# Kernel optimization log

Measured on AMD Instinct MI355X. Metric: run time of the kernel, lower is better.

Reference implementation:

```python
import jax, jax.numpy as jnp
import numpy as np

EMBED_DIM = 1024
NUM_HEADS = 16
HEAD_DIM = EMBED_DIM // NUM_HEADS
B, S = 2, 2048


def setup_inputs() -> dict:
    key = jax.random.key(0)
    ks = jax.random.split(key, 10)
    inp = {
        "query": jax.random.normal(ks[0], (B, S, EMBED_DIM), dtype=jnp.float32),
        "key": jax.random.normal(ks[1], (B, S, EMBED_DIM), dtype=jnp.float32),
        "value": jax.random.normal(ks[2], (B, S, EMBED_DIM), dtype=jnp.float32),
        # 0 => masked key position (matches attn_mask == 0 in the torch code)
        "attn_mask": jax.random.randint(ks[3], (B, S), 0, 2, dtype=jnp.int32),
        "Wq": jax.random.normal(ks[4], (EMBED_DIM, EMBED_DIM), dtype=jnp.float32) * 0.02,
        "bq": jnp.zeros((EMBED_DIM,), dtype=jnp.float32),
        "Wk": jax.random.normal(ks[5], (EMBED_DIM, EMBED_DIM), dtype=jnp.float32) * 0.02,
        "bk": jnp.zeros((EMBED_DIM,), dtype=jnp.float32),
        "Wv": jax.random.normal(ks[6], (EMBED_DIM, EMBED_DIM), dtype=jnp.float32) * 0.02,
        "bv": jnp.zeros((EMBED_DIM,), dtype=jnp.float32),
    }
    return inp


def _proj_heads(x, W, b):
    # x: [B, S, E] -> [B, H, S, D]  (nn.Linear uses x @ W.T + b)
    y = x @ W.T + b
    Bx, Sx, E = y.shape
    return y.reshape(Bx, Sx, NUM_HEADS, HEAD_DIM).transpose(0, 2, 1, 3)


def reference(query, key, value, attn_mask, Wq, bq, Wk, bk, Wv, bv):
    q = _proj_heads(query, Wq, bq)   # [B,H,S,D]
    k = _proj_heads(key, Wk, bk)     # [B,H,S,D]
    v = _proj_heads(value, Wv, bv)   # [B,H,S,D]
    inv_scale = float(EMBED_DIM) ** 0.5  # NOTE: original divides by sqrt(embed_dim), not sqrt(head_dim)
    scores = jnp.einsum("bhqd,bhkd->bhqk", q, k) / inv_scale  # [B,H,S,S]
    mask = (attn_mask == 0)[:, None, None, :]  # [B,1,1,S] -> broadcast over [B,H,S,S]
    scores = jnp.where(mask, -jnp.inf, scores)
    attn = jax.nn.softmax(scores, axis=-1)
    # dropout omitted for deterministic reference (see notes)
    out = jnp.einsum("bhqk,bhkd->bhqd", attn, v)  # [B,H,S,D]
    return out
```

## Files before the change

kernel.cpp:

```cpp
#include <hip/hip_runtime.h>
#include <hip/hip_bf16.h>

constexpr int BB = 2;
constexpr int SS = 2048;
constexpr int EE = 1024;
constexpr int HH = 16;
constexpr int DD = 64;
constexpr int MM = BB * SS;
constexpr int CX = MM * EE;
constexpr int CW = EE * EE;
#define QSCALE 0.045084220027780106f
#define NEGBIG -1e30f

typedef __attribute__((ext_vector_type(8))) short short8;
typedef __attribute__((ext_vector_type(4))) float floatx4;

__device__ inline short bf16bits(float x) {
    __hip_bfloat16 h = __float2bfloat16(x);
    return *reinterpret_cast<short*>(&h);
}

__device__ inline unsigned pkbf(float a, float b) {
    return (unsigned)(unsigned short)bf16bits(a) |
           ((unsigned)(unsigned short)bf16bits(b) << 16);
}

__device__ inline float fast_exp2(float x) {
#if __has_builtin(__builtin_amdgcn_exp2f)
    return __builtin_amdgcn_exp2f(x);
#else
    return exp2f(x);
#endif
}

__device__ inline void gl_lds16(const __hip_bfloat16* g, const short* l) {
    __builtin_amdgcn_global_load_lds(
        (const __attribute__((address_space(1))) void*)g,
        (__attribute__((address_space(3))) void*)l, 16, 0, 0);
}

__global__ __launch_bounds__(256) void convert_kernel(
    const float* __restrict__ x0, const float* __restrict__ x1, const float* __restrict__ x2,
    const float* __restrict__ w0, const float* __restrict__ w1, const float* __restrict__ w2,
    __hip_bfloat16* __restrict__ xb, __hip_bfloat16* __restrict__ wb)
{
    const long long e = (long long)(blockIdx.x * 256 + threadIdx.x) * 8;
    const float* src;
    __hip_bfloat16* dst;
    if (e < 3LL * CX) {
        const int z = (int)(e >> 22);
        const int off = (int)(e & (CX - 1));
        src = ((z == 0) ? x0 : (z == 1) ? x1 : x2) + off;
        dst = xb + e;
    } else {
        const long long e2 = e - 3LL * CX;
        const int z = (int)(e2 >> 20);
        const int off = (int)(e2 & (CW - 1));
        src = ((z == 0) ? w0 : (z == 1) ? w1 : w2) + off;
        dst = wb + e2;
    }
    const float4 a = reinterpret_cast<const float4*>(src)[0];
    const float4 b = reinterpret_cast<const float4*>(src)[1];
    short8 r;
    r[0] = bf16bits(a.x); r[1] = bf16bits(a.y); r[2] = bf16bits(a.z); r[3] = bf16bits(a.w);
    r[4] = bf16bits(b.x); r[5] = bf16bits(b.y); r[6] = bf16bits(b.z); r[7] = bf16bits(b.w);
    *reinterpret_cast<short8*>(dst) = r;
}

__global__ __launch_bounds__(256) void proj_gemm(
    const __hip_bfloat16* __restrict__ xb,
    const __hip_bfloat16* __restrict__ wb,
    const float* __restrict__ bq, const float* __restrict__ bk, const float* __restrict__ bv,
    __hip_bfloat16* __restrict__ qws,
    __hip_bfloat16* __restrict__ kws,
    __hip_bfloat16* __restrict__ vtws)
{
    const int which = blockIdx.z;
    const __hip_bfloat16* A = xb + (size_t)which * CX;
    const __hip_bfloat16* W = wb + (size_t)which * CW;
    const float* bias = (which == 0) ? bq : (which == 1) ? bk : bv;

    const int m0   = blockIdx.x * 128;
    const int n0   = blockIdx.y * 128;
    const int tid  = threadIdx.x;
    const int wave = tid >> 6;
    const int lane = tid & 63;
    const int l15  = lane & 15;
    const int quad = lane >> 4;
    const int wr   = wave >> 1;
    const int wc   = wave & 1;

    __shared__ __align__(16) short As[128 * 32];
    __shared__ __align__(16) short Bs[128 * 32];

    const int dpos  = (lane & 7) ^ (lane >> 3);
    const int drloc = 2 * (lane >> 3) + (dpos >> 2);
    const int dgran = (dpos & 3) * 8;

    const int rbase = (l15 >> 1) * 64;
    const int rslot = (((l15 & 1) * 4 + quad) ^ (l15 >> 1)) * 8;

    floatx4 acc[4][4] = {};

    for (int k0 = 0; k0 < EE; k0 += 32) {
        __syncthreads();
        #pragma unroll
        for (int p = 0; p < 2; ++p) {
            const int rb16 = wave * 32 + p * 16;
            gl_lds16(A + (size_t)(m0 + rb16 + drloc) * EE + k0 + dgran, &As[rb16 * 32]);
            gl_lds16(W + (size_t)(n0 + rb16 + drloc) * EE + k0 + dgran, &Bs[rb16 * 32]);
        }
        __syncthreads();

        short8 af[4], bf[4];
        #pragma unroll
        for (int mt = 0; mt < 4; ++mt)
            af[mt] = *reinterpret_cast<const short8*>(
                &As[(wr * 32 + mt * 8) * 64 + rbase + rslot]);
        #pragma unroll
        for (int nt = 0; nt < 4; ++nt)
            bf[nt] = *reinterpret_cast<const short8*>(
                &Bs[(wc * 32 + nt * 8) * 64 + rbase + rslot]);

        #pragma unroll
        for (int mt = 0; mt < 4; ++mt)
            #pragma unroll
            for (int nt = 0; nt < 4; ++nt)
                acc[mt][nt] = __builtin_amdgcn_mfma_f32_16x16x32_bf16(af[mt], bf[nt], acc[mt][nt], 0, 0, 0);
    }

    #pragma unroll
    for (int nt = 0; nt < 4; ++nt) {
        const int n = n0 + wc * 64 + nt * 16 + l15;
        const float bval = bias[n];
        const int h = n >> 6, d = n & 63;
        #pragma unroll
        for (int mt = 0; mt < 4; ++mt) {
            #pragma unroll
            for (int r = 0; r < 4; ++r) {
                const int m = m0 + wr * 64 + mt * 16 + quad * 4 + r;
                const int b = m >> 11;
                const int s = m & (SS - 1);
                float val = acc[mt][nt][r] + bval;
                if (which == 0) val *= QSCALE;
                const __hip_bfloat16 hv = __float2bfloat16(val);
                if (which == 0)
                    qws[(((size_t)b * HH + h) * SS + s) * DD + d] = hv;
                else if (which == 1)
                    kws[(((size_t)b * HH + h) * SS + s) * DD + d] = hv;
                else
                    vtws[(((size_t)b * HH + h) * DD + d) * SS + s] = hv;
            }
        }
    }
}

__global__ __launch_bounds__(256) void attn_kernel(
    const __hip_bfloat16* __restrict__ qws,
    const __hip_bfloat16* __restrict__ kws,
    const __hip_bfloat16* __restrict__ vtws,
    const int* __restrict__ amask,
    float* __restrict__ out)
{
    const int flatb = blockIdx.y * gridDim.x + blockIdx.x;
    const int bh    = 4 * (flatb & 7) + ((flatb >> 3) & 3);
    const int b     = bh >> 4;
    const int q0    = (flatb >> 5) * 64;
    const int tid  = threadIdx.x;
    const int wave = tid >> 6;
    const int lane = tid & 63;
    const int l15  = lane & 15;
    const int quad = lane >> 4;

    const __hip_bfloat16* Q  = qws  + (size_t)bh * SS * DD;
    const __hip_bfloat16* K  = kws  + (size_t)bh * SS * DD;
    const __hip_bfloat16* VT = vtws + (size_t)bh * DD * SS;
    const int* msk = amask + b * SS;

    __shared__ __align__(16) short Ks[64 * 64];
    __shared__ __align__(16) short Vs[64 * 64];
    __shared__ __align__(16) short Ps[4][16 * 64];
    short* pw = Ps[wave];

    const int qrow = q0 + wave * 16 + l15;
    const short8 qa0 = *reinterpret_cast<const short8*>(Q + (size_t)qrow * DD + quad * 8);
    const short8 qa1 = *reinterpret_cast<const short8*>(Q + (size_t)qrow * DD + 32 + quad * 8);

    const int swz = l15 & 7;

    const int srow = lane >> 3;
    const int sg   = ((lane & 7) ^ srow) * 8;

    float l_lane = 0.f;
    floatx4 acc[4] = {};

    for (int kt = 0; kt < SS; kt += 64) {
        __syncthreads();

        #pragma unroll
        for (int p = 0; p < 2; ++p) {
            const int rb = wave * 16 + p * 8;
            gl_lds16(K + (size_t)(kt + rb + srow) * DD + sg, &Ks[rb * 64]);
            gl_lds16(VT + (size_t)(rb + srow) * SS + kt + sg, &Vs[rb * 64]);
        }
        __syncthreads();

        floatx4 st[4];
        #pragma unroll
        for (int f = 0; f < 4; ++f) {
            const int krow = (f * 16 + l15) * 64;
            const short8 ka = *reinterpret_cast<const short8*>(&Ks[krow + (quad ^ swz) * 8]);
            const short8 kb = *reinterpret_cast<const short8*>(&Ks[krow + ((quad + 4) ^ swz) * 8]);
            floatx4 z = {};
            z = __builtin_amdgcn_mfma_f32_16x16x32_bf16(ka, qa0, z, 0, 0, 0);
            z = __builtin_amdgcn_mfma_f32_16x16x32_bf16(kb, qa1, z, 0, 0, 0);
            st[f] = z;
        }

        #pragma unroll
        for (int f = 0; f < 4; ++f) {
            const int4 mi = *reinterpret_cast<const int4*>(msk + kt + f * 16 + quad * 4);
            st[f][0] = fast_exp2(st[f][0] + (mi.x ? 0.f : NEGBIG));
            st[f][1] = fast_exp2(st[f][1] + (mi.y ? 0.f : NEGBIG));
            st[f][2] = fast_exp2(st[f][2] + (mi.z ? 0.f : NEGBIG));
            st[f][3] = fast_exp2(st[f][3] + (mi.w ? 0.f : NEGBIG));
            l_lane += st[f][0] + st[f][1] + st[f][2] + st[f][3];
        }

        #pragma unroll
        for (int f = 0; f < 4; ++f) {
            const int slot = (2 * f + (quad >> 1)) ^ swz;
            uint2 pk;
            pk.x = pkbf(st[f][0], st[f][1]);
            pk.y = pkbf(st[f][2], st[f][3]);
            *reinterpret_cast<uint2*>(pw + l15 * 64 + slot * 8 + (quad & 1) * 4) = pk;
        }
        __asm__ volatile("s_waitcnt lgkmcnt(0)" ::: "memory");

        const short8 pa0 = *reinterpret_cast<const short8*>(pw + l15 * 64 + (quad ^ swz) * 8);
        const short8 pa1 = *reinterpret_cast<const short8*>(pw + l15 * 64 + ((quad + 4) ^ swz) * 8);

        #pragma unroll
        for (int nt = 0; nt < 4; ++nt) {
            const int vrow = (nt * 16 + l15) * 64;
            const short8 vb0 = *reinterpret_cast<const short8*>(&Vs[vrow + (quad ^ swz) * 8]);
            const short8 vb1 = *reinterpret_cast<const short8*>(&Vs[vrow + ((quad + 4) ^ swz) * 8]);
            acc[nt] = __builtin_amdgcn_mfma_f32_16x16x32_bf16(pa0, vb0, acc[nt], 0, 0, 0);
            acc[nt] = __builtin_amdgcn_mfma_f32_16x16x32_bf16(pa1, vb1, acc[nt], 0, 0, 0);
        }
    }

    l_lane += __shfl_xor(l_lane, 16, 64);
    l_lane += __shfl_xor(l_lane, 32, 64);
    float lq[4];
    #pragma unroll
    for (int r = 0; r < 4; ++r)
        lq[r] = __shfl(l_lane, quad * 4 + r, 16);

    const size_t obase = (size_t)bh * SS * DD;
    #pragma unroll
    for (int nt = 0; nt < 4; ++nt)
        #pragma unroll
        for (int r = 0; r < 4; ++r) {
            const int qq = q0 + wave * 16 + quad * 4 + r;
            const int d  = nt * 16 + l15;
            out[obase + (size_t)qq * DD + d] = acc[nt][r] / lq[r];
        }
}

extern "C" void kernel_launch(void* const* d_in, const int* in_sizes, int n_in,
                              void* d_out, int out_size, void* d_ws, size_t ws_size,
                              hipStream_t stream) {
    const float* q    = (const float*)d_in[0];
    const float* k    = (const float*)d_in[1];
    const float* v    = (const float*)d_in[2];
    const int*   mask = (const int*)d_in[3];
    const float* Wq   = (const float*)d_in[4];
    const float* bq   = (const float*)d_in[5];
    const float* Wk   = (const float*)d_in[6];
    const float* bk   = (const float*)d_in[7];
    const float* Wv   = (const float*)d_in[8];
    const float* bv   = (const float*)d_in[9];
    float* out = (float*)d_out;

    __hip_bfloat16* qws  = (__hip_bfloat16*)d_ws;
    __hip_bfloat16* kws  = qws + (size_t)CX;
    __hip_bfloat16* vtws = kws + (size_t)CX;
    __hip_bfloat16* xb   = vtws + (size_t)CX;
    __hip_bfloat16* wb   = xb + (size_t)3 * CX;

    const int cvt_blocks = (3 * CX + 3 * CW) / (256 * 8);
    convert_kernel<<<dim3(cvt_blocks), 256, 0, stream>>>(q, k, v, Wq, Wk, Wv, xb, wb);
    proj_gemm<<<dim3(MM / 128, EE / 128, 3), 256, 0, stream>>>(
        xb, wb, bq, bk, bv, qws, kws, vtws);
    attn_kernel<<<dim3(SS / 64, BB * HH), 256, 0, stream>>>(
        qws, kws, vtws, mask, out);
}
```

Baseline: 215.1 us.

## Double-buffer K/V tiles, widen attention block to 128 queries, precompute mask in LDS

The attention kernel now handles 128 query rows per block, with each wave owning 32 rows, so every K/V tile loaded into LDS is reused twice as much and the grid is halved. K and V tiles are double-buffered, so the next tile's global-to-LDS copy overlaps compute on the current one, with one barrier per iteration instead of two. The mask is converted once to floats in LDS and applied as a multiply after exp2 instead of a select with a large negative bias, and setprio hints are added around the MFMA sections. In exchange the kernel uses more LDS and registers per block and launches fewer blocks, which may lower occupancy.

```diff
diff --git a/kernel.cpp b/kernel.cpp
--- a/kernel.cpp
+++ b/kernel.cpp
@@ -10,7 +10,6 @@
 constexpr int CX = MM * EE;
 constexpr int CW = EE * EE;
 #define QSCALE 0.045084220027780106f
-#define NEGBIG -1e30f
 
 typedef __attribute__((ext_vector_type(8))) short short8;
 typedef __attribute__((ext_vector_type(4))) float floatx4;
@@ -165,7 +164,7 @@
     const int flatb = blockIdx.y * gridDim.x + blockIdx.x;
     const int bh    = 4 * (flatb & 7) + ((flatb >> 3) & 3);
     const int b     = bh >> 4;
-    const int q0    = (flatb >> 5) * 64;
+    const int q0    = (flatb >> 5) * 128;
     const int tid  = threadIdx.x;
     const int wave = tid >> 6;
     const int lane = tid & 63;
@@ -177,94 +176,140 @@
     const __hip_bfloat16* VT = vtws + (size_t)bh * DD * SS;
     const int* msk = amask + b * SS;
 
-    __shared__ __align__(16) short Ks[64 * 64];
-    __shared__ __align__(16) short Vs[64 * 64];
-    __shared__ __align__(16) short Ps[4][16 * 64];
-    short* pw = Ps[wave];
-
-    const int qrow = q0 + wave * 16 + l15;
+    __shared__ __align__(16) short Ks[2][64 * 64];
+    __shared__ __align__(16) short Vs[2][64 * 64];
+    __shared__ __align__(16) short Ps[4][32 * 64];
+    __shared__ __align__(16) float Ms[SS];
+    short* pw0 = Ps[wave];
+    short* pw1 = Ps[wave] + 16 * 64;
+
+    #pragma unroll
+    for (int i = 0; i < 2; ++i) {
+        const int j = tid + i * 256;
+        const int4 m4 = reinterpret_cast<const int4*>(msk)[j];
+        float4 f4;
+        f4.x = (float)m4.x; f4.y = (float)m4.y; f4.z = (float)m4.z; f4.w = (float)m4.w;
+        reinterpret_cast<float4*>(Ms)[j] = f4;
+    }
+
+    const int qrow = q0 + wave * 32 + l15;
     const short8 qa0 = *reinterpret_cast<const short8*>(Q + (size_t)qrow * DD + quad * 8);
     const short8 qa1 = *reinterpret_cast<const short8*>(Q + (size_t)qrow * DD + 32 + quad * 8);
+    const short8 qa2 = *reinterpret_cast<const short8*>(Q + (size_t)(qrow + 16) * DD + quad * 8);
+    const short8 qa3 = *reinterpret_cast<const short8*>(Q + (size_t)(qrow + 16) * DD + 32 + quad * 8);
 
     const int swz = l15 & 7;
 
     const int srow = lane >> 3;
     const int sg   = ((lane & 7) ^ srow) * 8;
 
-    float l_lane = 0.f;
-    floatx4 acc[4] = {};
-
-    for (int kt = 0; kt < SS; kt += 64) {
-        __syncthreads();
-
-        #pragma unroll
-        for (int p = 0; p < 2; ++p) {
-            const int rb = wave * 16 + p * 8;
-            gl_lds16(K + (size_t)(kt + rb + srow) * DD + sg, &Ks[rb * 64]);
-            gl_lds16(VT + (size_t)(rb + srow) * SS + kt + sg, &Vs[rb * 64]);
-        }
-        __syncthreads();
-
-        floatx4 st[4];
+    float l0 = 0.f, l1 = 0.f;
+    floatx4 acc0[4] = {}, acc1[4] = {};
+
+    #pragma unroll
+    for (int p = 0; p < 2; ++p) {
+        const int rb = wave * 16 + p * 8;
+        gl_lds16(K + (size_t)(rb + srow) * DD + sg, &Ks[0][rb * 64]);
+        gl_lds16(VT + (size_t)(rb + srow) * SS + sg, &Vs[0][rb * 64]);
+    }
+    __asm__ volatile("s_waitcnt vmcnt(0) lgkmcnt(0)" ::: "memory");
+    __builtin_amdgcn_s_barrier();
+
+    for (int t = 0; t < SS / 64; ++t) {
+        const int cur = t & 1;
+
+        if (t + 1 < SS / 64) {
+            const int kn = (t + 1) * 64;
+            #pragma unroll
+            for (int p = 0; p < 2; ++p) {
+                const int rb = wave * 16 + p * 8;
+                gl_lds16(K + (size_t)(kn + rb + srow) * DD + sg, &Ks[cur ^ 1][rb * 64]);
+                gl_lds16(VT + (size_t)(rb + srow) * SS + kn + sg, &Vs[cur ^ 1][rb * 64]);
+            }
+        }
+        const int kt = t * 64;
+
+        floatx4 s0[4], s1[4];
+        __builtin_amdgcn_s_setprio(1);
         #pragma unroll
         for (int f = 0; f < 4; ++f) {
             const int krow = (f * 16 + l15) * 64;
-            const short8 ka = *reinterpret_cast<const short8*>(&Ks[krow + (quad ^ swz) * 8]);
-            const short8 kb = *reinterpret_cast<const short8*>(&Ks[krow + ((quad + 4) ^ swz) * 8]);
+            const short8 ka = *reinterpret_cast<const short8*>(&Ks[cur][krow + (quad ^ swz) * 8]);
+            const short8 kb = *reinterpret_cast<const short8*>(&Ks[cur][krow + ((quad + 4) ^ swz) * 8]);
             floatx4 z = {};
             z = __builtin_amdgcn_mfma_f32_16x16x32_bf16(ka, qa0, z, 0, 0, 0);
             z = __builtin_amdgcn_mfma_f32_16x16x32_bf16(kb, qa1, z, 0, 0, 0);
-            st[f] = z;
-        }
+            s0[f] = z;
+            floatx4 w = {};
+            w = __builtin_amdgcn_mfma_f32_16x16x32_bf16(ka, qa2, w, 0, 0, 0);
+            w = __builtin_amdgcn_mfma_f32_16x16x32_bf16(kb, qa3, w, 0, 0, 0);
+            s1[f] = w;
+        }
+        __builtin_amdgcn_s_setprio(0);
 
         #pragma unroll
         for (int f = 0; f < 4; ++f) {
-            const int4 mi = *reinterpret_cast<const int4*>(msk + kt + f * 16 + quad * 4);
-            st[f][0] = fast_exp2(st[f][0] + (mi.x ? 0.f : NEGBIG));
-            st[f][1] = fast_exp2(st[f][1] + (mi.y ? 0.f : NEGBIG));
-            st[f][2] = fast_exp2(st[f][2] + (mi.z ? 0.f : NEGBIG));
-            st[f][3] = fast_exp2(st[f][3] + (mi.w ? 0.f : NEGBIG));
-            l_lane += st[f][0] + st[f][1] + st[f][2] + st[f][3];
-        }
-
-        #pragma unroll
-        for (int f = 0; f < 4; ++f) {
-            const int slot = (2 * f + (quad >> 1)) ^ swz;
-            uint2 pk;
-            pk.x = pkbf(st[f][0], st[f][1]);
-            pk.y = pkbf(st[f][2], st[f][3]);
-            *reinterpret_cast<uint2*>(pw + l15 * 64 + slot * 8 + (quad & 1) * 4) = pk;
+            const float4 mf = *reinterpret_cast<const float4*>(&Ms[kt + f * 16 + quad * 4]);
+            const float e00 = fast_exp2(s0[f][0]) * mf.x;
+            const float e01 = fast_exp2(s0[f][1]) * mf.y;
+            const float e02 = fast_exp2(s0[f][2]) * mf.z;
+            const float e03 = fast_exp2(s0[f][3]) * mf.w;
+            const float e10 = fast_exp2(s1[f][0]) * mf.x;
+            const float e11 = fast_exp2(s1[f][1]) * mf.y;
+            const float e12 = fast_exp2(s1[f][2]) * mf.z;
+            const float e13 = fast_exp2(s1[f][3]) * mf.w;
+            l0 += e00 + e01 + e02 + e03;
+            l1 += e10 + e11 + e12 + e13;
+            const int slot = ((2 * f + (quad >> 1)) ^ swz) * 8 + (quad & 1) * 4;
+            uint2 p0; p0.x = pkbf(e00, e01); p0.y = pkbf(e02, e03);
+            uint2 p1; p1.x = pkbf(e10, e11); p1.y = pkbf(e12, e13);
+            *reinterpret_cast<uint2*>(pw0 + l15 * 64 + slot) = p0;
+            *reinterpret_cast<uint2*>(pw1 + l15 * 64 + slot) = p1;
         }
         __asm__ volatile("s_waitcnt lgkmcnt(0)" ::: "memory");
 
-        const short8 pa0 = *reinterpret_cast<const short8*>(pw + l15 * 64 + (quad ^ swz) * 8);
-        const short8 pa1 = *reinterpret_cast<const short8*>(pw + l15 * 64 + ((quad + 4) ^ swz) * 8);
-
+        const short8 pa0 = *reinterpret_cast<const short8*>(pw0 + l15 * 64 + (quad ^ swz) * 8);
+        const short8 pa1 = *reinterpret_cast<const short8*>(pw0 + l15 * 64 + ((quad + 4) ^ swz) * 8);
+        const short8 pb0 = *reinterpret_cast<const short8*>(pw1 + l15 * 64 + (quad ^ swz) * 8);
+        const short8 pb1 = *reinterpret_cast<const short8*>(pw1 + l15 * 64 + ((quad + 4) ^ swz) * 8);
+
+        __builtin_amdgcn_s_setprio(1);
         #pragma unroll
         for (int nt = 0; nt < 4; ++nt) {
             const int vrow = (nt * 16 + l15) * 64;
-            const short8 vb0 = *reinterpret_cast<const short8*>(&Vs[vrow + (quad ^ swz) * 8]);
-            const short8 vb1 = *reinterpret_cast<const short8*>(&Vs[vrow + ((quad + 4) ^ swz) * 8]);
-            acc[nt] = __builtin_amdgcn_mfma_f32_16x16x32_bf16(pa0, vb0, acc[nt], 0, 0, 0);
-            acc[nt] = __builtin_amdgcn_mfma_f32_16x16x32_bf16(pa1, vb1, acc[nt], 0, 0, 0);
-        }
-    }
-
-    l_lane += __shfl_xor(l_lane, 16, 64);
-    l_lane += __shfl_xor(l_lane, 32, 64);
-    float lq[4];
-    #pragma unroll
-    for (int r = 0; r < 4; ++r)
-        lq[r] = __shfl(l_lane, quad * 4 + r, 16);
+            const short8 vb0 = *reinterpret_cast<const short8*>(&Vs[cur][vrow + (quad ^ swz) * 8]);
+            const short8 vb1 = *reinterpret_cast<const short8*>(&Vs[cur][vrow + ((quad + 4) ^ swz) * 8]);
+            acc0[nt] = __builtin_amdgcn_mfma_f32_16x16x32_bf16(pa0, vb0, acc0[nt], 0, 0, 0);
+            acc0[nt] = __builtin_amdgcn_mfma_f32_16x16x32_bf16(pa1, vb1, acc0[nt], 0, 0, 0);
+            acc1[nt] = __builtin_amdgcn_mfma_f32_16x16x32_bf16(pb0, vb0, acc1[nt], 0, 0, 0);
+            acc1[nt] = __builtin_amdgcn_mfma_f32_16x16x32_bf16(pb1, vb1, acc1[nt], 0, 0, 0);
+        }
+        __builtin_amdgcn_s_setprio(0);
+
+        if (t + 1 < SS / 64) {
+            __asm__ volatile("s_waitcnt vmcnt(0)" ::: "memory");
+            __builtin_amdgcn_s_barrier();
+        }
+    }
+
+    l0 += __shfl_xor(l0, 16, 64); l0 += __shfl_xor(l0, 32, 64);
+    l1 += __shfl_xor(l1, 16, 64); l1 += __shfl_xor(l1, 32, 64);
+    float i0[4], i1[4];
+    #pragma unroll
+    for (int r = 0; r < 4; ++r) {
+        i0[r] = 1.f / __shfl(l0, quad * 4 + r, 16);
+        i1[r] = 1.f / __shfl(l1, quad * 4 + r, 16);
+    }
 
     const size_t obase = (size_t)bh * SS * DD;
     #pragma unroll
     for (int nt = 0; nt < 4; ++nt)
         #pragma unroll
         for (int r = 0; r < 4; ++r) {
-            const int qq = q0 + wave * 16 + quad * 4 + r;
+            const int qq = q0 + wave * 32 + quad * 4 + r;
             const int d  = nt * 16 + l15;
-            out[obase + (size_t)qq * DD + d] = acc[nt][r] / lq[r];
+            out[obase + (size_t)qq * DD + d] = acc0[nt][r] * i0[r];
+            out[obase + (size_t)(qq + 16) * DD + d] = acc1[nt][r] * i1[r];
         }
 }
 
@@ -293,6 +338,6 @@
     convert_kernel<<<dim3(cvt_blocks), 256, 0, stream>>>(q, k, v, Wq, Wk, Wv, xb, wb);
     proj_gemm<<<dim3(MM / 128, EE / 128, 3), 256, 0, stream>>>(
         xb, wb, bq, bk, bv, qws, kws, vtws);
-    attn_kernel<<<dim3(SS / 64, BB * HH), 256, 0, stream>>>(
+    attn_kernel<<<dim3(SS / 128, BB * HH), 256, 0, stream>>>(
         qws, kws, vtws, mask, out);
 }
```

Measured after the change: 211.1 us. About the same (-1.9%).
